# Kernel optimization log

Measured on AMD Instinct MI355X. Metric: run time of the kernel, lower is better.

The kernel has to match this reference:

```python
import jax, jax.numpy as jnp
import numpy as np


def _masked_var(x, mask):
    # unbiased variance (torch.var default, ddof=1) over entries where mask==1
    cnt = jnp.sum(mask)
    mean = jnp.sum(x * mask) / jnp.maximum(cnt, 1.0)
    return jnp.sum(mask * (x - mean) ** 2) / jnp.maximum(cnt - 1.0, 1.0)


def setup_inputs() -> dict:
    key = jax.random.key(0)
    ks = jax.random.split(key, 9)
    B, N, F = 4, 8192, 64
    points = jax.random.normal(ks[0], (B, N, 3), dtype=jnp.float32)
    features = jax.random.normal(ks[1], (B, N, F), dtype=jnp.float32)
    leaf_mask = jax.random.randint(ks[2], (B, N), 0, 2).astype(bool)
    W1 = jax.random.normal(ks[3], (64, F + 3), dtype=jnp.float32) * 0.05
    b1 = jax.random.normal(ks[4], (64,), dtype=jnp.float32) * 0.05
    W2 = jax.random.normal(ks[5], (32, 64), dtype=jnp.float32) * 0.05
    b2 = jax.random.normal(ks[6], (32,), dtype=jnp.float32) * 0.05
    W3 = jax.random.normal(ks[7], (1, 32), dtype=jnp.float32) * 0.05
    b3 = jax.random.normal(ks[8], (1,), dtype=jnp.float32) * 0.05
    return {"points": points, "features": features, "leaf_mask": leaf_mask,
            "W1": W1, "b1": b1, "W2": W2, "b2": b2, "W3": W3, "b3": b3}


def reference(points, features, leaf_mask, W1, b1, W2, b2, W3, b3):
    # NOTE: in the original Torch code combined_feat = [feat(F), xyz(3), var(1)]
    # (length F+4) is truncated to expected_input_dim = F+3, so the kNN feature
    # variance is provably dropped. The MLP input is exactly [feat, xyz].
    B, N, _ = points.shape

    def mlp(x):  # x: [N, F+3]
        h = jax.nn.relu(x @ W1.T + b1)
        h = jax.nn.relu(h @ W2.T + b2)
        return jax.nn.sigmoid(h @ W3.T + b3)[:, 0]

    def per_batch(pts, feats, mask):
        maskf = mask.astype(pts.dtype)
        x = jnp.concatenate([feats, pts], axis=-1)  # [N, F+3]
        scores = mlp(x) * maskf  # non-leaf points stay 0
        n_leaf = jnp.sum(maskf)
        scores = jnp.where(n_leaf < 10.0, jnp.zeros_like(scores), scores)

        # separation confidence
        clarity = _masked_var(scores, maskf)
        sel = scores > 0.7
        cnt = jnp.sum(sel.astype(jnp.int32))
        idx = jnp.arange(N)
        order = jnp.argsort(jnp.where(sel, idx, N + idx))  # selected first, in order
        g = pts[order]  # [N,3]
        d = jnp.linalg.norm(g[1:] - g[:-1], axis=1)  # consecutive boundary-point dists
        pair_mask = (jnp.arange(N - 1) < cnt - 1).astype(pts.dtype)
        dvar = _masked_var(d, pair_mask)
        cont = jnp.clip(1.0 / (dvar + 1e-8), 0.0, 1.0)
        cont = jnp.where(cnt > 5, cont, 0.0)
        conf = jnp.clip(clarity * cont, 0.0, 1.0)
        conf = jnp.where(n_leaf == 0.0, 0.0, conf)
        return scores, conf

    boundary_prob, separation_confidence = jax.vmap(per_batch)(points, features, leaf_mask)
    return boundary_prob, features, separation_confidence
```

## Files before the change

### kernel.cpp

```cpp
#include <hip/hip_runtime.h>
#include <math.h>

#define NB 4
#define NPTS 8192
#define OUT_FEAT_OFF 32768
#define OUT_CONF_OFF (32768 + 2097152)

__device__ __forceinline__ float blockReduceSum256(float v) {
    __shared__ float sred[4];
#pragma unroll
    for (int o = 32; o > 0; o >>= 1) v += __shfl_down(v, o, 64);
    const int w = threadIdx.x >> 6, l = threadIdx.x & 63;
    __syncthreads();
    if (l == 0) sred[w] = v;
    __syncthreads();
    return sred[0] + sred[1] + sred[2] + sred[3];
}

__global__ __launch_bounds__(256, 2) void fused_kernel(
    const float* __restrict__ pts,
    const float* __restrict__ feats,
    const int* __restrict__ mask,
    const float* __restrict__ W1,
    const float* __restrict__ b1,
    const float* __restrict__ W2,
    const float* __restrict__ b2,
    const float* __restrict__ W3,
    const float* __restrict__ b3,
    float* __restrict__ out,
    int* __restrict__ counters,
    float* __restrict__ wsf)
{
    __shared__ float smem[11264];
    float* const sX = smem;
    float* const sH = smem + 64 * 68;
    __shared__ int sflag;
    __shared__ int swt[4];

    const int t = threadIdx.x;
    const int ln = t & 63;
    const int q = __builtin_amdgcn_readfirstlane(t >> 6);

    const int p = blockIdx.x * 64 + ln;

    const float px = pts[(size_t)p * 3 + 0];
    const float py = pts[(size_t)p * 3 + 1];
    const float pz = pts[(size_t)p * 3 + 2];

    {
        const float4* fsrc = (const float4*)feats + (size_t)blockIdx.x * 1024;
        float4* fdst = (float4*)(out + OUT_FEAT_OFF) + (size_t)blockIdx.x * 1024;
#pragma unroll
        for (int i = 0; i < 4; ++i) {
            const int e = i * 256 + t;
            const float4 v = fsrc[e];
            fdst[e] = v;
            *(float4*)&sX[(e >> 4) * 68 + (e & 15) * 4] = v;
        }
    }
    __syncthreads();

    float4 xv[16];
#pragma unroll
    for (int kc = 0; kc < 16; ++kc)
        xv[kc] = *(const float4*)&sX[ln * 68 + kc * 4];

    const int jq = q * 16;
    float h1[16];
#pragma unroll
    for (int jj = 0; jj < 16; ++jj) {
        const float* __restrict__ wr = W1 + (size_t)(jq + jj) * 67;
        float a0 = b1[jq + jj], a1 = 0.f, a2 = 0.f, a3 = 0.f;
#pragma unroll
        for (int kc = 0; kc < 16; ++kc) {
            a0 = fmaf(xv[kc].x, wr[4 * kc + 0], a0);
            a1 = fmaf(xv[kc].y, wr[4 * kc + 1], a1);
            a2 = fmaf(xv[kc].z, wr[4 * kc + 2], a2);
            a3 = fmaf(xv[kc].w, wr[4 * kc + 3], a3);
        }
        a0 = fmaf(px, wr[64], a0);
        a1 = fmaf(py, wr[65], a1);
        a2 = fmaf(pz, wr[66], a2);
        h1[jj] = fmaxf((a0 + a1) + (a2 + a3), 0.f);
    }

    float p2[32];
#pragma unroll
    for (int j = 0; j < 32; ++j) {
        const float* __restrict__ wr = W2 + (size_t)j * 64 + jq;
        float a0 = 0.f, a1 = 0.f;
#pragma unroll
        for (int kk = 0; kk < 8; ++kk) {
            a0 = fmaf(h1[2 * kk + 0], wr[2 * kk + 0], a0);
            a1 = fmaf(h1[2 * kk + 1], wr[2 * kk + 1], a1);
        }
        p2[j] = a0 + a1;
    }

    if (q != 0) {
        float* dst = &sH[(size_t)((q - 1) * 64 + ln) * 36];
#pragma unroll
        for (int m = 0; m < 8; ++m) {
            float4 v;
            v.x = p2[4 * m + 0]; v.y = p2[4 * m + 1];
            v.z = p2[4 * m + 2]; v.w = p2[4 * m + 3];
            *(float4*)&dst[4 * m] = v;
        }
    }
    __syncthreads();

    if (q == 0) {
#pragma unroll
        for (int qq = 0; qq < 3; ++qq) {
            const float* src = &sH[(size_t)(qq * 64 + ln) * 36];
#pragma unroll
            for (int m = 0; m < 8; ++m) {
                const float4 v = *(const float4*)&src[4 * m];
                p2[4 * m + 0] += v.x; p2[4 * m + 1] += v.y;
                p2[4 * m + 2] += v.z; p2[4 * m + 3] += v.w;
            }
        }
        float z = b3[0];
#pragma unroll
        for (int j = 0; j < 32; ++j)
            z = fmaf(fmaxf(p2[j] + b2[j], 0.f), W3[j], z);
        float sc = 1.0f / (1.0f + expf(-z));
        if (mask[p] == 0) sc = 0.0f;
        out[p] = sc;
    }

    const int batch = blockIdx.x >> 7;
    __syncthreads();
    if (t == 0) {
        const int old = __hip_atomic_fetch_add(&counters[batch], 1,
                                               __ATOMIC_ACQ_REL,
                                               __HIP_MEMORY_SCOPE_AGENT);
        sflag = (old == 127);
    }
    __syncthreads();
    if (!sflag) return;
    __builtin_amdgcn_fence(__ATOMIC_ACQUIRE, "agent");

    float* scores = out + (size_t)batch * NPTS;
    const float* P = pts + (size_t)batch * NPTS * 3;
    const int* M = mask + (size_t)batch * NPTS;
    float* g = wsf + (size_t)batch * 40960;

    float s[32];
    unsigned int mbits = 0;
#pragma unroll
    for (int i = 0; i < 8; ++i) {
        const float4 s4 = ((const float4*)scores)[t * 8 + i];
        s[4*i+0] = s4.x; s[4*i+1] = s4.y; s[4*i+2] = s4.z; s[4*i+3] = s4.w;
        const int4 m4 = ((const int4*)M)[t * 8 + i];
        mbits |= (m4.x != 0 ? 1u : 0u) << (4*i+0);
        mbits |= (m4.y != 0 ? 1u : 0u) << (4*i+1);
        mbits |= (m4.z != 0 ? 1u : 0u) << (4*i+2);
        mbits |= (m4.w != 0 ? 1u : 0u) << (4*i+3);
    }

    float ss = 0.f;
#pragma unroll
    for (int i = 0; i < 32; ++i) ss += s[i];
    const float nleaf = blockReduceSum256((float)__popc(mbits));
    const float ssum = blockReduceSum256(ss);

    if (nleaf < 10.0f) {
        const float4 z4 = {0.f, 0.f, 0.f, 0.f};
#pragma unroll
        for (int i = 0; i < 8; ++i) ((float4*)scores)[t * 8 + i] = z4;
        if (t == 0) out[OUT_CONF_OFF + batch] = 0.0f;
        return;
    }

    const float mean = ssum / fmaxf(nleaf, 1.0f);
    float vs = 0.f;
#pragma unroll
    for (int i = 0; i < 32; ++i) {
        if (mbits & (1u << i)) {
            const float d0 = s[i] - mean;
            vs += d0 * d0;
        }
    }
    const float clarity = blockReduceSum256(vs) / fmaxf(nleaf - 1.0f, 1.0f);

    int c0 = 0;
#pragma unroll
    for (int i = 0; i < 32; ++i) c0 += (s[i] > 0.7f);
    int incl = c0;
#pragma unroll
    for (int o = 1; o < 64; o <<= 1) {
        const int u = __shfl_up(incl, o, 64);
        if (ln >= o) incl += u;
    }
    const int w = t >> 6;
    if (ln == 63) swt[w] = incl;
    __syncthreads();
    int woff = 0, cnt = 0;
#pragma unroll
    for (int i = 0; i < 4; ++i) {
        const int wv = swt[i];
        if (i < w) woff += wv;
        cnt += wv;
    }
    int pos = woff + (incl - c0);
#pragma unroll
    for (int i = 0; i < 32; ++i) {
        if (s[i] > 0.7f) {
            const int idx = t * 32 + i;
            g[3 * pos + 0] = P[3 * idx + 0];
            g[3 * pos + 1] = P[3 * idx + 1];
            g[3 * pos + 2] = P[3 * idx + 2];
            ++pos;
        }
    }
    __syncthreads();

    float* const ddl = smem;
    const int npair = cnt - 1;
    float dsum = 0.f;
#pragma unroll 4
    for (int i = t; i < npair; i += 256) {
        const float ax = g[3 * i + 0] - g[3 * i + 3];
        const float ay = g[3 * i + 1] - g[3 * i + 4];
        const float az = g[3 * i + 2] - g[3 * i + 5];
        const float d0 = sqrtf(ax * ax + ay * ay + az * az);
        ddl[i] = d0;
        dsum += d0;
    }
    const float dtot = blockReduceSum256(dsum);
    const float npf = (float)npair;
    const float dmean = dtot / fmaxf(npf, 1.0f);
    float dv = 0.f;
#pragma unroll 4
    for (int i = t; i < npair; i += 256) {
        const float e = ddl[i] - dmean;
        dv += e * e;
    }
    const float dvar = blockReduceSum256(dv) / fmaxf(npf - 1.0f, 1.0f);

    float cont = fminf(fmaxf(1.0f / (dvar + 1e-8f), 0.0f), 1.0f);
    if (!(cnt > 5)) cont = 0.0f;
    const float conf = fminf(fmaxf(clarity * cont, 0.0f), 1.0f);
    if (t == 0) out[OUT_CONF_OFF + batch] = conf;
}

extern "C" void kernel_launch(void* const* d_in, const int* in_sizes, int n_in,
                              void* d_out, int out_size, void* d_ws, size_t ws_size,
                              hipStream_t stream) {
    const float* points   = (const float*)d_in[0];
    const float* features = (const float*)d_in[1];
    const int*   leafmask = (const int*)d_in[2];
    const float* W1 = (const float*)d_in[3];
    const float* b1 = (const float*)d_in[4];
    const float* W2 = (const float*)d_in[5];
    const float* b2 = (const float*)d_in[6];
    const float* W3 = (const float*)d_in[7];
    const float* b3 = (const float*)d_in[8];
    float* out = (float*)d_out;
    int* counters = (int*)d_ws;
    float* wsf = (float*)d_ws + 64;

    (void)hipMemsetAsync(d_ws, 0, 64, stream);
    fused_kernel<<<512, 256, 0, stream>>>(
        points, features, leafmask, W1, b1, W2, b2, W3, b3, out, counters, wsf);
}
```

Baseline: 109.6 us.

## Remap MLP so lanes own neurons with register-resident weights

Restructures the per-point MLP so each lane holds one W1 row (and half of a W2 row) in registers while each wave walks 16 points read as LDS broadcasts. Hidden activations are staged in LDS, and layer-2 and layer-3 sums are reduced with cross-lane shuffles, replacing the per-point-per-lane scheme with scalar weight loads and a cross-wave partial-sum merge. The goal is to cut repeated weight fetches and the LDS reduction between waves. In exchange it adds shuffle chains, serial per-point loops and higher VGPR pressure (about 100 weight registers).

```diff
diff --git a/kernel.cpp b/kernel.cpp
--- a/kernel.cpp
+++ b/kernel.cpp
@@ -31,21 +31,35 @@
     int* __restrict__ counters,
     float* __restrict__ wsf)
 {
-    __shared__ float smem[11264];
+    __shared__ float smem[8704];
     float* const sX = smem;
-    float* const sH = smem + 64 * 68;
+    float* const sH1 = smem + 4352;
     __shared__ int sflag;
     __shared__ int swt[4];
 
     const int t = threadIdx.x;
     const int ln = t & 63;
-    const int q = __builtin_amdgcn_readfirstlane(t >> 6);
-
-    const int p = blockIdx.x * 64 + ln;
-
-    const float px = pts[(size_t)p * 3 + 0];
-    const float py = pts[(size_t)p * 3 + 1];
-    const float pz = pts[(size_t)p * 3 + 2];
+    const int w = __builtin_amdgcn_readfirstlane(t >> 6);
+    const int prow = w * 16;
+
+    float wv1[67];
+#pragma unroll
+    for (int k = 0; k < 67; ++k) wv1[k] = W1[ln * 67 + k];
+    const float b1v = b1[ln];
+    const int j2 = ln & 31, kh = ln >> 5;
+    float wv2[32];
+    {
+        const float* w2r = W2 + j2 * 64 + (kh << 5);
+#pragma unroll
+        for (int m = 0; m < 8; ++m) {
+            const float4 v = *(const float4*)&w2r[4 * m];
+            wv2[4*m+0] = v.x; wv2[4*m+1] = v.y;
+            wv2[4*m+2] = v.z; wv2[4*m+3] = v.w;
+        }
+    }
+    const float b2v = b2[j2];
+    const float w3v = W3[j2];
+    const float b3v = b3[0];
 
     {
         const float4* fsrc = (const float4*)feats + (size_t)blockIdx.x * 1024;
@@ -57,76 +71,63 @@
             fdst[e] = v;
             *(float4*)&sX[(e >> 4) * 68 + (e & 15) * 4] = v;
         }
-    }
-    __syncthreads();
-
-    float4 xv[16];
-#pragma unroll
-    for (int kc = 0; kc < 16; ++kc)
-        xv[kc] = *(const float4*)&sX[ln * 68 + kc * 4];
-
-    const int jq = q * 16;
-    float h1[16];
-#pragma unroll
-    for (int jj = 0; jj < 16; ++jj) {
-        const float* __restrict__ wr = W1 + (size_t)(jq + jj) * 67;
-        float a0 = b1[jq + jj], a1 = 0.f, a2 = 0.f, a3 = 0.f;
-#pragma unroll
-        for (int kc = 0; kc < 16; ++kc) {
-            a0 = fmaf(xv[kc].x, wr[4 * kc + 0], a0);
-            a1 = fmaf(xv[kc].y, wr[4 * kc + 1], a1);
-            a2 = fmaf(xv[kc].z, wr[4 * kc + 2], a2);
-            a3 = fmaf(xv[kc].w, wr[4 * kc + 3], a3);
-        }
-        a0 = fmaf(px, wr[64], a0);
-        a1 = fmaf(py, wr[65], a1);
-        a2 = fmaf(pz, wr[66], a2);
-        h1[jj] = fmaxf((a0 + a1) + (a2 + a3), 0.f);
-    }
-
-    float p2[32];
-#pragma unroll
-    for (int j = 0; j < 32; ++j) {
-        const float* __restrict__ wr = W2 + (size_t)j * 64 + jq;
+        if (t < 192) {
+            const float v = pts[(size_t)blockIdx.x * 192 + t];
+            sX[(t / 3) * 68 + 64 + (t % 3)] = v;
+        }
+    }
+    __syncthreads();
+
+#pragma unroll 4
+    for (int p = 0; p < 16; ++p) {
+        const float* xr = &sX[(prow + p) * 68];
+        float4 xq[17];
+#pragma unroll
+        for (int c = 0; c < 17; ++c) xq[c] = *(const float4*)&xr[4 * c];
+        float a0 = b1v, a1 = 0.f, a2 = 0.f, a3 = 0.f;
+#pragma unroll
+        for (int c = 0; c < 16; ++c) {
+            a0 = fmaf(xq[c].x, wv1[4 * c + 0], a0);
+            a1 = fmaf(xq[c].y, wv1[4 * c + 1], a1);
+            a2 = fmaf(xq[c].z, wv1[4 * c + 2], a2);
+            a3 = fmaf(xq[c].w, wv1[4 * c + 3], a3);
+        }
+        a0 = fmaf(xq[16].x, wv1[64], a0);
+        a1 = fmaf(xq[16].y, wv1[65], a1);
+        a2 = fmaf(xq[16].z, wv1[66], a2);
+        const float h = fmaxf((a0 + a1) + (a2 + a3), 0.f);
+        sH1[(prow + p) * 68 + ln] = h;
+    }
+
+    float zkeep = 0.f;
+#pragma unroll 4
+    for (int p = 0; p < 16; ++p) {
+        const float* hr = &sH1[(prow + p) * 68 + (kh << 5)];
         float a0 = 0.f, a1 = 0.f;
 #pragma unroll
-        for (int kk = 0; kk < 8; ++kk) {
-            a0 = fmaf(h1[2 * kk + 0], wr[2 * kk + 0], a0);
-            a1 = fmaf(h1[2 * kk + 1], wr[2 * kk + 1], a1);
-        }
-        p2[j] = a0 + a1;
-    }
-
-    if (q != 0) {
-        float* dst = &sH[(size_t)((q - 1) * 64 + ln) * 36];
-#pragma unroll
         for (int m = 0; m < 8; ++m) {
-            float4 v;
-            v.x = p2[4 * m + 0]; v.y = p2[4 * m + 1];
-            v.z = p2[4 * m + 2]; v.w = p2[4 * m + 3];
-            *(float4*)&dst[4 * m] = v;
-        }
-    }
-    __syncthreads();
-
-    if (q == 0) {
-#pragma unroll
-        for (int qq = 0; qq < 3; ++qq) {
-            const float* src = &sH[(size_t)(qq * 64 + ln) * 36];
-#pragma unroll
-            for (int m = 0; m < 8; ++m) {
-                const float4 v = *(const float4*)&src[4 * m];
-                p2[4 * m + 0] += v.x; p2[4 * m + 1] += v.y;
-                p2[4 * m + 2] += v.z; p2[4 * m + 3] += v.w;
-            }
-        }
-        float z = b3[0];
-#pragma unroll
-        for (int j = 0; j < 32; ++j)
-            z = fmaf(fmaxf(p2[j] + b2[j], 0.f), W3[j], z);
-        float sc = 1.0f / (1.0f + expf(-z));
-        if (mask[p] == 0) sc = 0.0f;
-        out[p] = sc;
+            const float4 v = *(const float4*)&hr[4 * m];
+            a0 = fmaf(v.x, wv2[4*m+0], a0);
+            a1 = fmaf(v.y, wv2[4*m+1], a1);
+            a0 = fmaf(v.z, wv2[4*m+2], a0);
+            a1 = fmaf(v.w, wv2[4*m+3], a1);
+        }
+        float hs = a0 + a1;
+        hs += __shfl_xor(hs, 32, 64);
+        float t3 = fmaxf(hs + b2v, 0.f) * w3v;
+        t3 += __shfl_xor(t3, 16, 64);
+        t3 += __shfl_xor(t3, 8, 64);
+        t3 += __shfl_xor(t3, 4, 64);
+        t3 += __shfl_xor(t3, 2, 64);
+        t3 += __shfl_xor(t3, 1, 64);
+        if (ln == p) zkeep = t3 + b3v;
+    }
+
+    if (ln < 16) {
+        const int pp = blockIdx.x * 64 + prow + ln;
+        float sc = 1.0f / (1.0f + expf(-zkeep));
+        if (mask[pp] == 0) sc = 0.0f;
+        out[pp] = sc;
     }
 
     const int batch = blockIdx.x >> 7;
@@ -193,15 +194,15 @@
         const int u = __shfl_up(incl, o, 64);
         if (ln >= o) incl += u;
     }
-    const int w = t >> 6;
-    if (ln == 63) swt[w] = incl;
+    const int wv = t >> 6;
+    if (ln == 63) swt[wv] = incl;
     __syncthreads();
     int woff = 0, cnt = 0;
 #pragma unroll
     for (int i = 0; i < 4; ++i) {
-        const int wv = swt[i];
-        if (i < w) woff += wv;
-        cnt += wv;
+        const int wt = swt[i];
+        if (i < wv) woff += wt;
+        cnt += wt;
     }
     int pos = woff + (incl - c0);
 #pragma unroll
```

Result: slower. 151.5 us (+38.2%).
